# Performance work log

Measured on AMD Instinct MI355X. Metric: run time of the kernel, lower is better.

The kernel has to match this reference:

```python
import jax, jax.numpy as jnp
import numpy as np

DIM = 512
H = 4
HD = DIM // H
NPL = 2  # num_proj_layers
PS = float(np.sqrt(0.1))  # prior_strength ** 0.5


def conv1d(x, w, b):
    # x: [B,C,L], w: [O,I,3], SAME padding
    y = jax.lax.conv_general_dilated(x, w, window_strides=(1,), padding=[(1, 1)],
                                     dimension_numbers=('NCH', 'OIH', 'NCH'))
    return y + b[None, :, None]


def layernorm(x, g, b):
    m = jnp.mean(x, -1, keepdims=True)
    v = jnp.var(x, -1, keepdims=True)
    return (x - m) * jax.lax.rsqrt(v + 1e-5) * g + b


def maxpool1d(x):
    # kernel 3, stride 2, pad 1 (padded with -inf, matching torch MaxPool1d)
    return jax.lax.reduce_window(x, -jnp.inf, jax.lax.max, (1, 1, 3), (1, 1, 2),
                                 ((0, 0), (0, 0), (1, 1)))


def ds_block(x, cw, cb, g, b):
    # silu(conv) -> LN over channels -> maxpool; x: [B,C,L]
    x = jax.nn.silu(conv1d(x, cw, cb))
    x = jnp.swapaxes(layernorm(jnp.swapaxes(x, 1, 2), g, b), 1, 2)
    return maxpool1d(x)


def replicate_pad_odd(x):
    # F.pad(x, (0,0,0,1), 'replicate')[:, 1::2] on [B,S,D]
    return jnp.concatenate([x, x[:, -1:]], axis=1)[:, 1::2]


def setup_inputs() -> dict:
    key = jax.random.key(0)
    ks = jax.random.split(key, 16)
    B, Sq, Skv, C = 8, 2048, 512, DIM

    def n(k, shp, s=0.02):
        return jax.random.normal(k, shp, jnp.float32) * s

    return {
        'q_x': jax.random.normal(ks[0], (B, Sq, C), jnp.float32),
        'kv_x': jax.random.normal(ks[1], (B, Skv, C), jnp.float32),
        'q_freqs_cis': jax.random.normal(ks[2], (B, Sq, HD), jnp.float32),
        'k_freqs_cis': jax.random.normal(ks[3], (B, Skv, HD), jnp.float32),
        'mask': jnp.zeros((B, 1, (Sq + 1) // 2, Skv), jnp.float32),
        'attn_prior': jax.random.uniform(ks[4], (B, Sq, Skv), jnp.float32),
        'qds_conv_w': n(ks[5], (C, C, 3), 0.05),
        'qds_conv_b': jnp.zeros((C,), jnp.float32),
        'qds_ln_g': jnp.ones((C,), jnp.float32),
        'qds_ln_b': jnp.zeros((C,), jnp.float32),
        'qp_conv_w': n(ks[6], (NPL, C, C, 3), 0.05),
        'qp_conv_b': jnp.zeros((NPL, C), jnp.float32),
        'qp_ln_g': jnp.ones((NPL, C), jnp.float32),
        'qp_ln_b': jnp.zeros((NPL, C), jnp.float32),
        'wq': n(ks[7], (C, C)),
        'wk': n(ks[8], (C, C)),
        'wv': n(ks[9], (C, C)),
        'score_w': n(ks[10], (H, H, 45, 5), 0.02),
        'score_b': jnp.zeros((H,), jnp.float32),
        'proj_w': n(ks[11], (C, C)),
        'proj_b': jnp.zeros((C,), jnp.float32),
    }


def reference(q_x, kv_x, q_freqs_cis, k_freqs_cis, mask, attn_prior,
              qds_conv_w, qds_conv_b, qds_ln_g, qds_ln_b,
              qp_conv_w, qp_conv_b, qp_ln_g, qp_ln_b,
              wq, wk, wv, score_w, score_b, proj_w, proj_b):
    B, Sq, C = q_x.shape
    Skv = kv_x.shape[1]
    scale = HD ** -0.5

    # QueryDownsample: length Sq -> (Sq+1)//2
    x = ds_block(jnp.swapaxes(q_x, 1, 2), qds_conv_w, qds_conv_b, qds_ln_g, qds_ln_b)

    # QueryProj (note: original loop `for i in range(1, num_layers)` never uses xs[num_layers])
    xs = [x]
    for i in range(NPL):
        x = ds_block(x, qp_conv_w[i], qp_conv_b[i], qp_ln_g[i], qp_ln_b[i])
        xs.append(x)
    out = xs[0]
    for i in range(1, NPL):
        xi = jnp.repeat(xs[i], 2 ** i, axis=-1)  # nearest upsample
        out = out + xi[..., :out.shape[-1]]
    qx = jnp.swapaxes(out, 1, 2)  # [B, Sq2, C]
    Sq2 = (Sq + 1) // 2

    q = (qx @ wq.T).reshape(B, Sq2, H, HD)
    k = (kv_x @ wk.T).reshape(B, Skv, H, HD)
    v = (kv_x @ wv.T).reshape(B, Skv, H, HD)

    qf = replicate_pad_odd(q_freqs_cis)  # [B, Sq2, HD]
    q = q + qf[:, :, None] * PS
    k = k + k_freqs_cis[:, :, None] * PS

    q = jnp.swapaxes(q, 1, 2)  # [B,H,Sq2,HD]
    k = jnp.swapaxes(k, 1, 2)
    v = jnp.swapaxes(v, 1, 2)

    # gaussian attention: negative clamped squared L2 distance
    qs = q * scale
    kk = k * scale
    x2 = jnp.sum(qs * qs, -1)  # [B,H,Sq2]
    y2 = jnp.sum(kk * kk, -1)  # [B,H,Skv]
    xy = jnp.einsum('bhid,bhjd->bhij', qs, kk)
    attn = -jnp.clip(x2[..., :, None] + y2[..., None, :] - 2.0 * xy, 0.0, None)

    temp = jnp.linspace(1.0, 10.0, H).astype(attn.dtype)
    attn = attn / temp[None, :, None, None]

    # Conv2d(H,H,(45,5),padding=(22,2)) over the score map (mixes heads)
    sc = jax.lax.conv_general_dilated(attn, score_w, (1, 1), ((22, 22), (2, 2)),
                                      dimension_numbers=('NCHW', 'OIHW', 'NCHW'))
    attn = attn + sc + score_b[None, :, None, None]
    attn = attn + mask
    attn = jax.nn.softmax(attn, axis=-1)

    # prior log-fusion + renormalize
    prior = replicate_pad_odd(attn_prior)  # [B,Sq2,Skv]
    attn = jnp.exp(jnp.log(jnp.clip(attn, 1e-8, None)) +
                   jnp.log(jnp.clip(prior[:, None], 1e-8, None)))
    attn = attn / (jnp.sum(attn, -1, keepdims=True) + 1e-8)

    # nearest interpolate (Sq2 -> 2*Sq2) then crop to Sq
    attn = jnp.repeat(attn, 2, axis=2)[:, :, :Sq]  # [B,H,Sq,Skv]

    xout = jnp.einsum('bhqk,bhkd->bhqd', attn, v)
    xout = jnp.swapaxes(xout, 1, 2).reshape(B, Sq, C)
    xout = xout @ proj_w.T + proj_b
    return xout, attn
```

## Files before the change

### kernel.cpp

```cpp
#include <hip/hip_runtime.h>
#include <math.h>

#define PS_CONST 0.31622776601683794f

typedef __attribute__((ext_vector_type(8))) short short8;
typedef __attribute__((ext_vector_type(4))) float f32x4;

__device__ inline unsigned short f2b(float f) {
    unsigned u = __builtin_bit_cast(unsigned, f);
    unsigned r = (u + 0x7fffu + ((u >> 16) & 1u)) >> 16;
    return (unsigned short)r;
}

__global__ __launch_bounds__(256) void cvt_bf16_k(const float* __restrict__ in,
                                                  ushort* __restrict__ out, int n4)
{
    int idx = blockIdx.x * 256 + threadIdx.x;
    if (idx >= n4) return;
    float4 vv = ((const float4*)in)[idx];
    ushort4 o;
    o.x = f2b(vv.x); o.y = f2b(vv.y); o.z = f2b(vv.z); o.w = f2b(vv.w);
    ((ushort4*)out)[idx] = o;
}

__global__ __launch_bounds__(256) void wcvt_k(const float* __restrict__ w,
                                              ushort* __restrict__ out)
{
    int idx = blockIdx.x * 256 + threadIdx.x;
    if (idx >= 786432) return;
    int c = idx / 1536;
    int rem = idx - c * 1536;
    int tap = rem >> 9, i = rem & 511;
    out[idx] = f2b(w[c * 1536 + i * 3 + tap]);
}

__global__ __launch_bounds__(256) void wcvt4_k(
    const float* __restrict__ w0, const float* __restrict__ w1,
    const float* __restrict__ w2, const float* __restrict__ w3,
    ushort* __restrict__ o0, ushort* __restrict__ o1,
    ushort* __restrict__ o2, ushort* __restrict__ o3)
{
    int idx = blockIdx.x * 256 + threadIdx.x;
    int sel = idx >> 16, off = idx & 65535;
    const float* w = (sel == 0) ? w0 : (sel == 1) ? w1 : (sel == 2) ? w2 : w3;
    ushort* o = (sel == 0) ? o0 : (sel == 1) ? o1 : (sel == 2) ? o2 : o3;
    float4 vv = ((const float4*)w)[off];
    ushort4 r;
    r.x = f2b(vv.x); r.y = f2b(vv.y); r.z = f2b(vv.z); r.w = f2b(vv.w);
    ((ushort4*)o)[off] = r;
}

__global__ __launch_bounds__(256) void atoep_k(const float* __restrict__ sw,
                                               ushort* __restrict__ At)
{
    int idx = blockIdx.x * 256 + threadIdx.x;
    if (idx >= 81920) return;
    int t = idx & 7;
    int lane = (idx >> 3) & 63;
    int ks = (idx >> 9) & 1;
    int rem = idx >> 10;
    int dj = rem % 5, ohi = rem / 5;
    int m = lane & 15;
    int k = ks * 32 + ((lane >> 4) << 3) + t;
    int d = k - m;
    float val = (d >= 0 && d < 45) ? sw[(ohi * 45 + d) * 5 + dj] : 0.f;
    At[idx] = f2b(val);
}

__global__ __launch_bounds__(256) void conv_mfma(
    const ushort* __restrict__ xtb, const ushort* __restrict__ wtb,
    const float* __restrict__ cb, float* __restrict__ z, int L)
{
    __shared__ __align__(16) ushort Ash[128 * 40];
    __shared__ __align__(16) ushort Bsh[128 * 40];
    const int b = blockIdx.z;
    const int cm = blockIdx.y << 7;
    const int l0 = blockIdx.x << 7;
    const int tid = threadIdx.x;
    const int wave = tid >> 6, lane = tid & 63;
    const int wm = (wave & 1) << 6, wn = (wave >> 1) << 6;
    const int lo16 = lane & 15, hi4 = lane >> 4;

    f32x4 acc[4][4];
    #pragma unroll
    for (int i = 0; i < 4; i++)
        #pragma unroll
        for (int j = 0; j < 4; j++)
            acc[i][j] = (f32x4){0.f, 0.f, 0.f, 0.f};

    for (int k0 = 0; k0 < 1536; k0 += 32) {
        const int tap = k0 >> 9;
        const int cbase = k0 & 511;
        {
            int u = tid;
            #pragma unroll
            for (int p = 0; p < 2; p++, u += 256) {
                int row = u >> 2, g = (u & 3) << 3;
                *(uint4*)&Ash[row * 40 + g] =
                    *(const uint4*)&wtb[(size_t)(cm + row) * 1536 + k0 + g];
            }
        }
        {
            int u = tid;
            #pragma unroll
            for (int p = 0; p < 2; p++, u += 256) {
                int row = u >> 2, g = (u & 3) << 3;
                int lg = l0 + tap - 1 + row;
                uint4 val = make_uint4(0u, 0u, 0u, 0u);
                if (lg >= 0 && lg < L)
                    val = *(const uint4*)&xtb[((size_t)b * L + lg) * 512 + cbase + g];
                *(uint4*)&Bsh[row * 40 + g] = val;
            }
        }
        __syncthreads();
        short8 a[4], bb[4];
        #pragma unroll
        for (int t = 0; t < 4; t++) {
            a[t]  = *(const short8*)&Ash[(wm + t * 16 + lo16) * 40 + hi4 * 8];
            bb[t] = *(const short8*)&Bsh[(wn + t * 16 + lo16) * 40 + hi4 * 8];
        }
        #pragma unroll
        for (int mt = 0; mt < 4; mt++)
            #pragma unroll
            for (int nt = 0; nt < 4; nt++)
                acc[mt][nt] = __builtin_amdgcn_mfma_f32_16x16x32_bf16(
                    a[mt], bb[nt], acc[mt][nt], 0, 0, 0);
        __syncthreads();
    }
    #pragma unroll
    for (int mt = 0; mt < 4; mt++) {
        #pragma unroll
        for (int r = 0; r < 4; r++) {
            int c = cm + wm + mt * 16 + hi4 * 4 + r;
            float bias = cb[c];
            #pragma unroll
            for (int nt = 0; nt < 4; nt++) {
                int l = l0 + wn + nt * 16 + lo16;
                float u = acc[mt][nt][r] + bias;
                u = u / (1.f + __expf(-u));
                z[((size_t)b * 512 + c) * L + l] = u;
            }
        }
    }
}

__global__ __launch_bounds__(256) void gemm_mfma_bf16(
    const ushort* __restrict__ Xb, const ushort* __restrict__ Wb,
    const float* __restrict__ bias, float* __restrict__ Y,
    int M, int N, int K, int dup)
{
    __shared__ __align__(16) ushort Ash[128 * 40];
    __shared__ __align__(16) ushort Bsh[128 * 40];
    const int bm = blockIdx.y << 7, bn = blockIdx.x << 7;
    const int tid = threadIdx.x;
    const int wave = tid >> 6, lane = tid & 63;
    const int wm = (wave & 1) << 6, wn = (wave >> 1) << 6;
    const int lo16 = lane & 15, hi4 = lane >> 4;

    f32x4 acc[4][4];
    #pragma unroll
    for (int i = 0; i < 4; i++)
        #pragma unroll
        for (int j = 0; j < 4; j++)
            acc[i][j] = (f32x4){0.f, 0.f, 0.f, 0.f};

    for (int k0 = 0; k0 < K; k0 += 32) {
        int u = tid;
        #pragma unroll
        for (int p = 0; p < 2; p++, u += 256) {
            int row = u >> 2, g = (u & 3) << 3;
            *(uint4*)&Ash[row * 40 + g] =
                *(const uint4*)&Xb[(size_t)(bm + row) * K + k0 + g];
            *(uint4*)&Bsh[row * 40 + g] =
                *(const uint4*)&Wb[(size_t)(bn + row) * K + k0 + g];
        }
        __syncthreads();
        short8 a[4], bb[4];
        #pragma unroll
        for (int t = 0; t < 4; t++) {
            a[t]  = *(const short8*)&Ash[(wm + t * 16 + lo16) * 40 + hi4 * 8];
            bb[t] = *(const short8*)&Bsh[(wn + t * 16 + lo16) * 40 + hi4 * 8];
        }
        #pragma unroll
        for (int mt = 0; mt < 4; mt++)
            #pragma unroll
            for (int nt = 0; nt < 4; nt++)
                acc[mt][nt] = __builtin_amdgcn_mfma_f32_16x16x32_bf16(
                    a[mt], bb[nt], acc[mt][nt], 0, 0, 0);
        __syncthreads();
    }
    #pragma unroll
    for (int mt = 0; mt < 4; mt++) {
        #pragma unroll
        for (int r = 0; r < 4; r++) {
            int m = bm + wm + mt * 16 + hi4 * 4 + r;
            #pragma unroll
            for (int nt = 0; nt < 4; nt++) {
                int n = bn + wn + nt * 16 + lo16;
                float val = acc[mt][nt][r];
                if (bias) val += bias[n];
                if (dup) {
                    Y[(size_t)(2 * m)     * N + n] = val;
                    Y[(size_t)(2 * m + 1) * N + n] = val;
                } else {
                    Y[(size_t)m * N + n] = val;
                }
            }
        }
    }
}

__global__ __launch_bounds__(256) void ln_stats_k(const float* __restrict__ z,
                                                  float2* __restrict__ stats, int L)
{
    __shared__ float s_sh[4][64];
    __shared__ float s2_sh[4][64];
    const int b = blockIdx.y;
    const int colL = threadIdx.x & 63;
    const int col = (blockIdx.x << 6) + colL;
    const int part = threadIdx.x >> 6;
    const float* base = z + ((size_t)b * 512 + part * 128) * L + col;
    float s = 0.f, s2 = 0.f;
    for (int i = 0; i < 128; i++) {
        float vv = base[(size_t)i * L];
        s += vv; s2 += vv * vv;
    }
    s_sh[part][colL] = s; s2_sh[part][colL] = s2;
    __syncthreads();
    if (threadIdx.x < 64) {
        float ts = 0.f, ts2 = 0.f;
        #pragma unroll
        for (int p = 0; p < 4; p++) { ts += s_sh[p][colL]; ts2 += s2_sh[p][colL]; }
        float m = ts * (1.f / 512.f);
        float var = ts2 * (1.f / 512.f) - m * m;
        stats[(size_t)b * L + col] = make_float2(m, rsqrtf(var + 1e-5f));
    }
}

__global__ __launch_bounds__(256) void ln_maxpool_k(
    const float* __restrict__ z, const float2* __restrict__ stats,
    const float* __restrict__ g, const float* __restrict__ be,
    float* __restrict__ out, int L, int lshift)
{
    const int Lout = 1 << lshift;
    size_t idx = (size_t)blockIdx.x * 256 + threadIdx.x;
    int lp = (int)(idx & (Lout - 1));
    int c = (int)((idx >> lshift) & 511);
    int b = (int)(idx >> (lshift + 9));
    const float* zp = z + ((size_t)b * 512 + c) * L;
    const float2* sp = stats + (size_t)b * L;
    float gc = g[c], bc = be[c];
    int l = lp << 1;
    float2 st = sp[l];
    float m = (zp[l] - st.x) * st.y * gc + bc;
    if (l > 0) {
        float2 s0 = sp[l - 1];
        m = fmaxf(m, (zp[l - 1] - s0.x) * s0.y * gc + bc);
    }
    float2 s1 = sp[l + 1];
    m = fmaxf(m, (zp[l + 1] - s1.x) * s1.y * gc + bc);
    out[idx] = m;
}

__global__ __launch_bounds__(256) void transpose_cvt_k(const float* __restrict__ x0,
                                                       ushort* __restrict__ xtb)
{
    __shared__ ushort t[32][33];
    const int b = blockIdx.z, c0 = blockIdx.y << 5, l0 = blockIdx.x << 5;
    const int col = threadIdx.x & 31, r0 = threadIdx.x >> 5;
    #pragma unroll
    for (int p = 0; p < 4; p++) {
        int r = r0 + p * 8;
        t[r][col] = f2b(x0[((size_t)b * 512 + c0 + r) * 1024 + l0 + col]);
    }
    __syncthreads();
    #pragma unroll
    for (int p = 0; p < 4; p++) {
        int r = r0 + p * 8;
        xtb[((size_t)b * 1024 + l0 + r) * 512 + c0 + col] = t[col][r];
    }
}

__global__ __launch_bounds__(256) void vT_cvt_k(const float* __restrict__ v,
                                                ushort* __restrict__ vTb)
{
    __shared__ ushort t[32][33];
    const int bh = blockIdx.z, b = bh >> 2, h = bh & 3;
    const int d0 = blockIdx.y << 5, j0 = blockIdx.x << 5;
    const int col = threadIdx.x & 31, r0 = threadIdx.x >> 5;
    #pragma unroll
    for (int p = 0; p < 4; p++) {
        int r = r0 + p * 8;
        t[r][col] = f2b(v[(((size_t)b * 512 + j0 + r) * 4 + h) * 128 + d0 + col]);
    }
    __syncthreads();
    #pragma unroll
    for (int p = 0; p < 4; p++) {
        int r = r0 + p * 8;
        vTb[((size_t)bh * 128 + d0 + r) * 512 + j0 + col] = t[col][r];
    }
}

__global__ __launch_bounds__(256) void upsample_add_t(const float* __restrict__ x0,
    const float* __restrict__ x1, ushort* __restrict__ qxb)
{
    size_t idx = (size_t)blockIdx.x * 256 + threadIdx.x;
    int c = (int)(idx & 511);
    int l = (int)((idx >> 9) & 1023);
    int b = (int)(idx >> 19);
    qxb[idx] = f2b(x0[((size_t)b * 512 + c) * 1024 + l] +
                   x1[((size_t)b * 512 + c) * 512 + (l >> 1)]);
}

__global__ __launch_bounds__(256) void add_freq_q_k(float* __restrict__ q, const float* __restrict__ qf)
{
    size_t idx = (size_t)blockIdx.x * 256 + threadIdx.x;
    int d = (int)(idx & 127);
    int l = (int)((idx >> 9) & 1023);
    int b = (int)(idx >> 19);
    q[idx] += PS_CONST * qf[((size_t)b * 2048 + 2 * l + 1) * 128 + d];
}

__global__ __launch_bounds__(256) void add_freq_k_k(float* __restrict__ k, const float* __restrict__ kf)
{
    size_t idx = (size_t)blockIdx.x * 256 + threadIdx.x;
    int d = (int)(idx & 127);
    int j = (int)((idx >> 9) & 511);
    int b = (int)(idx >> 18);
    k[idx] += PS_CONST * kf[((size_t)b * 512 + j) * 128 + d];
}

__global__ __launch_bounds__(64) void rownorm_k(const float* __restrict__ X,
                                                float* __restrict__ out, int Li)
{
    int i = blockIdx.x, bh = blockIdx.y;
    int b = bh >> 2, h = bh & 3;
    const float* row = X + (((size_t)b * Li + i) * 4 + h) * 128;
    int lane = threadIdx.x;
    float v0 = row[lane], v1 = row[lane + 64];
    float s = v0 * v0 + v1 * v1;
    #pragma unroll
    for (int off = 32; off > 0; off >>= 1) s += __shfl_down(s, off);
    if (lane == 0) out[(size_t)bh * Li + i] = s;
}

__global__ __launch_bounds__(256) void scores_k(
    const float* __restrict__ q, const float* __restrict__ k,
    const float* __restrict__ q2, const float* __restrict__ k2,
    float* __restrict__ attn0)
{
    __shared__ float As[16][68];
    __shared__ float Bs[16][68];
    const int bh = blockIdx.z, b = bh >> 2, h = bh & 3;
    const float* A  = q + (size_t)b * (1024 * 512) + h * 128;
    const float* Bm = k + (size_t)b * (512 * 512) + h * 128;
    const int bm = blockIdx.y << 6, bn = blockIdx.x << 6;
    const int tx = threadIdx.x & 15, ty = threadIdx.x >> 4;
    const int lrow = threadIdx.x >> 2, lkc = (threadIdx.x & 3) << 2;
    float acc[4][4] = {};
    for (int k0 = 0; k0 < 128; k0 += 16) {
        float4 a4 = *(const float4*)&A[(size_t)(bm + lrow) * 512 + k0 + lkc];
        float4 b4 = *(const float4*)&Bm[(size_t)(bn + lrow) * 512 + k0 + lkc];
        As[lkc+0][lrow] = a4.x; As[lkc+1][lrow] = a4.y; As[lkc+2][lrow] = a4.z; As[lkc+3][lrow] = a4.w;
        Bs[lkc+0][lrow] = b4.x; Bs[lkc+1][lrow] = b4.y; Bs[lkc+2][lrow] = b4.z; Bs[lkc+3][lrow] = b4.w;
        __syncthreads();
        #pragma unroll
        for (int kk = 0; kk < 16; kk++) {
            float4 a4v = *(const float4*)&As[kk][ty << 2];
            float4 b4v = *(const float4*)&Bs[kk][tx << 2];
            float a[4] = {a4v.x, a4v.y, a4v.z, a4v.w};
            float bb[4] = {b4v.x, b4v.y, b4v.z, b4v.w};
            #pragma unroll
            for (int u = 0; u < 4; u++)
                #pragma unroll
                for (int vv = 0; vv < 4; vv++)
                    acc[u][vv] = fmaf(a[u], bb[vv], acc[u][vv]);
        }
        __syncthreads();
    }
    const float it = (h == 0) ? 1.f : (h == 1) ? 0.25f : (h == 2) ? (1.f / 7.f) : 0.1f;
    float* orow = attn0 + (size_t)bh * (1024 * 512);
    #pragma unroll
    for (int u = 0; u < 4; u++) {
        int i = bm + (ty << 2) + u;
        float q2v = q2[(size_t)bh * 1024 + i];
        #pragma unroll
        for (int vv = 0; vv < 4; vv++) {
            int j = bn + (tx << 2) + vv;
            float d2 = q2v + k2[(size_t)bh * 512 + j] - 2.f * acc[u][vv];
            d2 *= (1.f / 128.f);
            if (d2 < 0.f) d2 = 0.f;
            orow[(size_t)i * 512 + j] = -d2 * it;
        }
    }
}

__global__ __launch_bounds__(256) void score_conv_mfma(
    const float* __restrict__ attn0, const ushort* __restrict__ At,
    const float* __restrict__ sb, const float* __restrict__ mask,
    float* __restrict__ attn1)
{
    __shared__ __align__(16) ushort tileT[4 * 68 * 120];
    const int b = blockIdx.z, i0 = blockIdx.y << 6, j0 = blockIdx.x << 6;
    const int tid = threadIdx.x, wave = tid >> 6, lane = tid & 63;

    for (int idx = tid; idx < 4 * 68 * 56; idx += 256) {
        int jj = idx % 68;
        int r2 = idx / 68;
        int ip = r2 % 56, hi = r2 / 56;
        int ii = ip << 1;
        int gi = i0 - 22 + ii, gj = j0 - 2 + jj;
        const float* src = attn0 + ((size_t)(b * 4 + hi) * 1024 + gi) * 512 + gj;
        bool jv = (unsigned)gj < 512u;
        float v0 = (jv && (unsigned)gi       < 1024u) ? src[0]   : 0.f;
        float v1 = (jv && (unsigned)(gi + 1) < 1024u) ? src[512] : 0.f;
        unsigned pk = (unsigned)f2b(v0) | ((unsigned)f2b(v1) << 16);
        *(unsigned*)&tileT[(hi * 68 + jj) * 120 + ii] = pk;
    }
    __syncthreads();

    const int n16 = lane & 15, quad = lane >> 4;
    f32x4 acc[4][4];
    #pragma unroll
    for (int o = 0; o < 4; o++)
        #pragma unroll
        for (int t = 0; t < 4; t++)
            acc[o][t] = (f32x4){0.f, 0.f, 0.f, 0.f};

    const int iibase = wave * 16 + quad * 8;
    #pragma unroll 1
    for (int hi = 0; hi < 4; hi++) {
        #pragma unroll 1
        for (int dj = 0; dj < 5; dj++) {
            #pragma unroll
            for (int ks = 0; ks < 2; ks++) {
                short8 bf[4];
                #pragma unroll
                for (int t = 0; t < 4; t++)
                    bf[t] = *(const short8*)&tileT[(hi * 68 + t * 16 + n16 + dj) * 120
                                                   + iibase + ks * 32];
                #pragma unroll
                for (int o = 0; o < 4; o++) {
                    short8 af = *(const short8*)&At[((((o * 4 + hi) * 5 + dj) * 2 + ks) * 64
                                                     + lane) * 8];
                    #pragma unroll
                    for (int t = 0; t < 4; t++)
                        acc[o][t] = __builtin_amdgcn_mfma_f32_16x16x32_bf16(
                            af, bf[t], acc[o][t], 0, 0, 0);
                }
            }
        }
    }

    #pragma unroll
    for (int o = 0; o < 4; o++) {
        float bo = sb[o];
        #pragma unroll
        for (int r = 0; r < 4; r++) {
            int i = i0 + wave * 16 + quad * 4 + r;
            size_t obase = ((size_t)(b * 4 + o) * 1024 + i) * 512;
            size_t mbase = ((size_t)b * 1024 + i) * 512;
            #pragma unroll
            for (int t = 0; t < 4; t++) {
                int j = j0 + t * 16 + n16;
                attn1[obase + j] = attn0[obase + j] + acc[o][t][r] + bo + mask[mbase + j];
            }
        }
    }
}

__global__ __launch_bounds__(256) void softmax_prior_k(
    const float* __restrict__ attn1, const float* __restrict__ prior,
    float* __restrict__ attn_out)
{
    const int wid = threadIdx.x >> 6, lane = threadIdx.x & 63;
    size_t row = (size_t)blockIdx.x * 4 + wid;
    int i = (int)(row & 1023);
    int bh = (int)(row >> 10);
    int b = bh >> 2;
    const float* arow = attn1 + row * 512;
    const float* prow = prior + ((size_t)b * 2048 + 2 * i + 1) * 512;
    float v[8], p[8];
    #pragma unroll
    for (int t = 0; t < 8; t++) {
        v[t] = arow[lane + 64 * t];
        p[t] = prow[lane + 64 * t];
    }
    float mx = v[0];
    #pragma unroll
    for (int t = 1; t < 8; t++) mx = fmaxf(mx, v[t]);
    #pragma unroll
    for (int off = 32; off > 0; off >>= 1) mx = fmaxf(mx, __shfl_xor(mx, off));
    float sum = 0.f;
    #pragma unroll
    for (int t = 0; t < 8; t++) { v[t] = expf(v[t] - mx); sum += v[t]; }
    #pragma unroll
    for (int off = 32; off > 0; off >>= 1) sum += __shfl_xor(sum, off);
    float inv = 1.f / sum;
    float sum2 = 0.f;
    #pragma unroll
    for (int t = 0; t < 8; t++) {
        float sm = fmaxf(v[t] * inv, 1e-8f);
        float pr = fmaxf(p[t], 1e-8f);
        v[t] = sm * pr;
        sum2 += v[t];
    }
    #pragma unroll
    for (int off = 32; off > 0; off >>= 1) sum2 += __shfl_xor(sum2, off);
    float inv2 = 1.f / (sum2 + 1e-8f);
    float* o0 = attn_out + ((size_t)bh * 2048 + 2 * i) * 512;
    #pragma unroll
    for (int t = 0; t < 8; t++) {
        float val = v[t] * inv2;
        o0[lane + 64 * t] = val;
        o0[512 + lane + 64 * t] = val;
    }
}

__global__ __launch_bounds__(256) void attnv_mfma(
    const float* __restrict__ attn, const ushort* __restrict__ vTb,
    ushort* __restrict__ xpb)
{
    __shared__ __align__(16) ushort Ash[128 * 40];
    __shared__ __align__(16) ushort Bsh[128 * 40];
    const int bh = blockIdx.z, b = bh >> 2, h = bh & 3;
    const int bm = blockIdx.y << 7;
    const float* A = attn + (size_t)bh * 2048 * 512;
    const ushort* B = vTb + (size_t)bh * 128 * 512;
    const int tid = threadIdx.x;
    const int wave = tid >> 6, lane = tid & 63;
    const int wm = (wave & 1) << 6, wn = (wave >> 1) << 6;
    const int lo16 = lane & 15, hi4 = lane >> 4;

    f32x4 acc[4][4];
    #pragma unroll
    for (int i = 0; i < 4; i++)
        #pragma unroll
        for (int j = 0; j < 4; j++)
            acc[i][j] = (f32x4){0.f, 0.f, 0.f, 0.f};

    for (int k0 = 0; k0 < 512; k0 += 32) {
        int u = tid;
        #pragma unroll
        for (int p = 0; p < 2; p++, u += 256) {
            int row = u >> 2, g = (u & 3) << 3;
            const float* ap = &A[(size_t)(2 * (bm + row)) * 512 + k0 + g];
            float4 f0 = *(const float4*)ap;
            float4 f1 = *(const float4*)(ap + 4);
            ushort4 p0, p1;
            p0.x = f2b(f0.x); p0.y = f2b(f0.y); p0.z = f2b(f0.z); p0.w = f2b(f0.w);
            p1.x = f2b(f1.x); p1.y = f2b(f1.y); p1.z = f2b(f1.z); p1.w = f2b(f1.w);
            *(ushort4*)&Ash[row * 40 + g]     = p0;
            *(ushort4*)&Ash[row * 40 + g + 4] = p1;
            *(uint4*)&Bsh[row * 40 + g] = *(const uint4*)&B[(size_t)row * 512 + k0 + g];
        }
        __syncthreads();
        short8 a[4], bb[4];
        #pragma unroll
        for (int t = 0; t < 4; t++) {
            a[t]  = *(const short8*)&Ash[(wm + t * 16 + lo16) * 40 + hi4 * 8];
            bb[t] = *(const short8*)&Bsh[(wn + t * 16 + lo16) * 40 + hi4 * 8];
        }
        #pragma unroll
        for (int mt = 0; mt < 4; mt++)
            #pragma unroll
            for (int nt = 0; nt < 4; nt++)
                acc[mt][nt] = __builtin_amdgcn_mfma_f32_16x16x32_bf16(
                    a[mt], bb[nt], acc[mt][nt], 0, 0, 0);
        __syncthreads();
    }
    #pragma unroll
    for (int mt = 0; mt < 4; mt++) {
        #pragma unroll
        for (int r = 0; r < 4; r++) {
            int m = bm + wm + mt * 16 + hi4 * 4 + r;
            #pragma unroll
            for (int nt = 0; nt < 4; nt++) {
                int n = wn + nt * 16 + lo16;
                xpb[((size_t)b * 1024 + m) * 512 + h * 128 + n] = f2b(acc[mt][nt][r]);
            }
        }
    }
}

extern "C" void kernel_launch(void* const* d_in, const int* in_sizes, int n_in,
                              void* d_out, int out_size, void* d_ws, size_t ws_size,
                              hipStream_t stream)
{
    const float* q_x    = (const float*)d_in[0];
    const float* kv_x   = (const float*)d_in[1];
    const float* qf     = (const float*)d_in[2];
    const float* kf     = (const float*)d_in[3];
    const float* mask   = (const float*)d_in[4];
    const float* prior  = (const float*)d_in[5];
    const float* qds_w  = (const float*)d_in[6];
    const float* qds_b  = (const float*)d_in[7];
    const float* qds_g  = (const float*)d_in[8];
    const float* qds_be = (const float*)d_in[9];
    const float* qp_w   = (const float*)d_in[10];
    const float* qp_b   = (const float*)d_in[11];
    const float* qp_g   = (const float*)d_in[12];
    const float* qp_be  = (const float*)d_in[13];
    const float* wq     = (const float*)d_in[14];
    const float* wk     = (const float*)d_in[15];
    const float* wv     = (const float*)d_in[16];
    const float* sw     = (const float*)d_in[17];
    const float* sb     = (const float*)d_in[18];
    const float* pw     = (const float*)d_in[19];
    const float* pb     = (const float*)d_in[20];

    if (ws_size < (size_t)56672256 * 4) return;
    float* ws = (float*)d_ws;
    float* z     = ws;
    float* x0    = ws + 8388608;
    float* x1    = ws + 12582912;
    float* q     = ws + 14680064;
    float* k     = ws + 18874368;
    float* v     = ws + 20971520;
    float* q2    = ws + 23068672;
    float* k2    = ws + 23101440;
    float* attn0 = ws + 23117824;
    float* attn1 = ws + 39895040;
    ushort* xtb   = (ushort*)(ws + 39895040);
    ushort* x0tb  = (ushort*)(ws + 39895040 + 4194304);
    ushort* wc1b  = (ushort*)(ws + 39895040 + 6291456);
    ushort* wc2b  = (ushort*)(ws + 39895040 + 6684672);
    float2* stats1 = (float2*)(ws + 39895040 + 7077888);
    float2* stats2 = (float2*)(ws + 39895040 + 7110656);
    ushort* qxb  = (ushort*)z;
    ushort* At   = (ushort*)x0;
    ushort* wqb  = (ushort*)(ws + 8454144);
    ushort* wkb  = (ushort*)(ws + 8585216);
    ushort* wvb  = (ushort*)(ws + 8716288);
    ushort* pwb  = (ushort*)(ws + 8847360);
    ushort* vTb  = (ushort*)(ws + 11010048);
    ushort* kvb  = (ushort*)x1;
    ushort* xpb  = (ushort*)attn0;

    float* out_x    = (float*)d_out;
    float* out_attn = out_x + (size_t)8 * 2048 * 512;

    cvt_bf16_k<<<8192, 256, 0, stream>>>(q_x, xtb, 2097152);
    wcvt_k<<<3072, 256, 0, stream>>>(qds_w, wc1b);
    wcvt_k<<<3072, 256, 0, stream>>>(qp_w, wc2b);
    conv_mfma<<<dim3(16, 4, 8), 256, 0, stream>>>(xtb, wc1b, qds_b, z, 2048);
    ln_stats_k<<<dim3(32, 8), 256, 0, stream>>>(z, stats1, 2048);
    ln_maxpool_k<<<16384, 256, 0, stream>>>(z, stats1, qds_g, qds_be, x0, 2048, 10);
    transpose_cvt_k<<<dim3(32, 16, 8), 256, 0, stream>>>(x0, x0tb);
    conv_mfma<<<dim3(8, 4, 8), 256, 0, stream>>>(x0tb, wc2b, qp_b, z, 1024);
    ln_stats_k<<<dim3(16, 8), 256, 0, stream>>>(z, stats2, 1024);
    ln_maxpool_k<<<8192, 256, 0, stream>>>(z, stats2, qp_g, qp_be, x1, 1024, 9);
    upsample_add_t<<<16384, 256, 0, stream>>>(x0, x1, qxb);
    atoep_k<<<320, 256, 0, stream>>>(sw, At);
    wcvt4_k<<<1024, 256, 0, stream>>>(wq, wk, wv, pw, wqb, wkb, wvb, pwb);
    cvt_bf16_k<<<2048, 256, 0, stream>>>(kv_x, kvb, 524288);
    gemm_mfma_bf16<<<dim3(4, 64), 256, 0, stream>>>(qxb, wqb, nullptr, q, 8192, 512, 512, 0);
    gemm_mfma_bf16<<<dim3(4, 32), 256, 0, stream>>>(kvb, wkb, nullptr, k, 4096, 512, 512, 0);
    gemm_mfma_bf16<<<dim3(4, 32), 256, 0, stream>>>(kvb, wvb, nullptr, v, 4096, 512, 512, 0);
    add_freq_q_k<<<16384, 256, 0, stream>>>(q, qf);
    add_freq_k_k<<<8192, 256, 0, stream>>>(k, kf);
    rownorm_k<<<dim3(1024, 32), 64, 0, stream>>>(q, q2, 1024);
    rownorm_k<<<dim3(512, 32), 64, 0, stream>>>(k, k2, 512);
    vT_cvt_k<<<dim3(16, 4, 32), 256, 0, stream>>>(v, vTb);
    scores_k<<<dim3(8, 16, 32), 256, 0, stream>>>(q, k, q2, k2, attn0);
    score_conv_mfma<<<dim3(8, 16, 8), 256, 0, stream>>>(attn0, At, sb, mask, attn1);
    softmax_prior_k<<<8192, 256, 0, stream>>>(attn1, prior, out_attn);
    attnv_mfma<<<dim3(1, 8, 32), 256, 0, stream>>>(out_attn, vTb, xpb);
    gemm_mfma_bf16<<<dim3(4, 64), 256, 0, stream>>>(xpb, pwb, pb, out_x, 8192, 512, 512, 1);
}
```

Baseline: 786.5 us.

## Compute distance scores with split-bf16 MFMA instead of scalar FP32 GEMM

```diff
diff --git a/kernel.cpp b/kernel.cpp
--- a/kernel.cpp
+++ b/kernel.cpp
@@ -10,6 +10,9 @@
     unsigned u = __builtin_bit_cast(unsigned, f);
     unsigned r = (u + 0x7fffu + ((u >> 16) & 1u)) >> 16;
     return (unsigned short)r;
+}
+__device__ inline float b2f(unsigned short b) {
+    return __builtin_bit_cast(float, (unsigned)b << 16);
 }
 
 __global__ __launch_bounds__(256) void cvt_bf16_k(const float* __restrict__ in,
@@ -21,6 +24,23 @@
     ushort4 o;
     o.x = f2b(vv.x); o.y = f2b(vv.y); o.z = f2b(vv.z); o.w = f2b(vv.w);
     ((ushort4*)out)[idx] = o;
+}
+
+__global__ __launch_bounds__(256) void split_bf16_k(const float* __restrict__ in,
+    ushort* __restrict__ hi, ushort* __restrict__ lo, int n4)
+{
+    int idx = blockIdx.x * 256 + threadIdx.x;
+    if (idx >= n4) return;
+    float4 vv = ((const float4*)in)[idx];
+    float vs[4] = {vv.x, vv.y, vv.z, vv.w};
+    ushort4 h, l;
+    unsigned short hb; float hf;
+    hb = f2b(vs[0]); hf = b2f(hb); h.x = hb; l.x = f2b(vs[0] - hf);
+    hb = f2b(vs[1]); hf = b2f(hb); h.y = hb; l.y = f2b(vs[1] - hf);
+    hb = f2b(vs[2]); hf = b2f(hb); h.z = hb; l.z = f2b(vs[2] - hf);
+    hb = f2b(vs[3]); hf = b2f(hb); h.w = hb; l.w = f2b(vs[3] - hf);
+    ((ushort4*)hi)[idx] = h;
+    ((ushort4*)lo)[idx] = l;
 }
 
 __global__ __launch_bounds__(256) void wcvt_k(const float* __restrict__ w,
@@ -344,53 +364,81 @@
     if (lane == 0) out[(size_t)bh * Li + i] = s;
 }
 
-__global__ __launch_bounds__(256) void scores_k(
-    const float* __restrict__ q, const float* __restrict__ k,
+__global__ __launch_bounds__(256) void scores_mfma(
+    const ushort* __restrict__ qhi, const ushort* __restrict__ qlo,
+    const ushort* __restrict__ khi, const ushort* __restrict__ klo,
     const float* __restrict__ q2, const float* __restrict__ k2,
     float* __restrict__ attn0)
 {
-    __shared__ float As[16][68];
-    __shared__ float Bs[16][68];
+    __shared__ __align__(16) ushort Ah[128 * 40];
+    __shared__ __align__(16) ushort Al[128 * 40];
+    __shared__ __align__(16) ushort Bh[128 * 40];
+    __shared__ __align__(16) ushort Bl[128 * 40];
     const int bh = blockIdx.z, b = bh >> 2, h = bh & 3;
-    const float* A  = q + (size_t)b * (1024 * 512) + h * 128;
-    const float* Bm = k + (size_t)b * (512 * 512) + h * 128;
-    const int bm = blockIdx.y << 6, bn = blockIdx.x << 6;
-    const int tx = threadIdx.x & 15, ty = threadIdx.x >> 4;
-    const int lrow = threadIdx.x >> 2, lkc = (threadIdx.x & 3) << 2;
-    float acc[4][4] = {};
-    for (int k0 = 0; k0 < 128; k0 += 16) {
-        float4 a4 = *(const float4*)&A[(size_t)(bm + lrow) * 512 + k0 + lkc];
-        float4 b4 = *(const float4*)&Bm[(size_t)(bn + lrow) * 512 + k0 + lkc];
-        As[lkc+0][lrow] = a4.x; As[lkc+1][lrow] = a4.y; As[lkc+2][lrow] = a4.z; As[lkc+3][lrow] = a4.w;
-        Bs[lkc+0][lrow] = b4.x; Bs[lkc+1][lrow] = b4.y; Bs[lkc+2][lrow] = b4.z; Bs[lkc+3][lrow] = b4.w;
+    const int bm = blockIdx.y << 7, bn = blockIdx.x << 7;
+    const int tid = threadIdx.x;
+    const int wave = tid >> 6, lane = tid & 63;
+    const int wm = (wave & 1) << 6, wn = (wave >> 1) << 6;
+    const int lo16 = lane & 15, hi4 = lane >> 4;
+
+    f32x4 acc[4][4];
+    #pragma unroll
+    for (int i = 0; i < 4; i++)
+        #pragma unroll
+        for (int j = 0; j < 4; j++)
+            acc[i][j] = (f32x4){0.f, 0.f, 0.f, 0.f};
+
+    for (int k0 = 0; k0 < 128; k0 += 32) {
+        int u = tid;
+        #pragma unroll
+        for (int p = 0; p < 2; p++, u += 256) {
+            int row = u >> 2, g = (u & 3) << 3;
+            size_t aoff = (((size_t)b * 1024 + bm + row) * 4 + h) * 128 + k0 + g;
+            size_t boff = (((size_t)b * 512  + bn + row) * 4 + h) * 128 + k0 + g;
+            *(uint4*)&Ah[row * 40 + g] = *(const uint4*)&qhi[aoff];
+            *(uint4*)&Al[row * 40 + g] = *(const uint4*)&qlo[aoff];
+            *(uint4*)&Bh[row * 40 + g] = *(const uint4*)&khi[boff];
+            *(uint4*)&Bl[row * 40 + g] = *(const uint4*)&klo[boff];
+        }
         __syncthreads();
-        #pragma unroll
-        for (int kk = 0; kk < 16; kk++) {
-            float4 a4v = *(const float4*)&As[kk][ty << 2];
-            float4 b4v = *(const float4*)&Bs[kk][tx << 2];
-            float a[4] = {a4v.x, a4v.y, a4v.z, a4v.w};
-            float bb[4] = {b4v.x, b4v.y, b4v.z, b4v.w};
-            #pragma unroll
-            for (int u = 0; u < 4; u++)
-                #pragma unroll
-                for (int vv = 0; vv < 4; vv++)
-                    acc[u][vv] = fmaf(a[u], bb[vv], acc[u][vv]);
-        }
+        short8 ah[4], al[4], bhF[4], blF[4];
+        #pragma unroll
+        for (int t = 0; t < 4; t++) {
+            int ar = (wm + t * 16 + lo16) * 40 + hi4 * 8;
+            int br = (wn + t * 16 + lo16) * 40 + hi4 * 8;
+            ah[t]  = *(const short8*)&Ah[ar];
+            al[t]  = *(const short8*)&Al[ar];
+            bhF[t] = *(const short8*)&Bh[br];
+            blF[t] = *(const short8*)&Bl[br];
+        }
+        #pragma unroll
+        for (int mt = 0; mt < 4; mt++)
+            #pragma unroll
+            for (int nt = 0; nt < 4; nt++) {
+                acc[mt][nt] = __builtin_amdgcn_mfma_f32_16x16x32_bf16(
+                    ah[mt], bhF[nt], acc[mt][nt], 0, 0, 0);
+                acc[mt][nt] = __builtin_amdgcn_mfma_f32_16x16x32_bf16(
+                    ah[mt], blF[nt], acc[mt][nt], 0, 0, 0);
+                acc[mt][nt] = __builtin_amdgcn_mfma_f32_16x16x32_bf16(
+                    al[mt], bhF[nt], acc[mt][nt], 0, 0, 0);
+            }
         __syncthreads();
     }
     const float it = (h == 0) ? 1.f : (h == 1) ? 0.25f : (h == 2) ? (1.f / 7.f) : 0.1f;
-    float* orow = attn0 + (size_t)bh * (1024 * 512);
-    #pragma unroll
-    for (int u = 0; u < 4; u++) {
-        int i = bm + (ty << 2) + u;
-        float q2v = q2[(size_t)bh * 1024 + i];
-        #pragma unroll
-        for (int vv = 0; vv < 4; vv++) {
-            int j = bn + (tx << 2) + vv;
-            float d2 = q2v + k2[(size_t)bh * 512 + j] - 2.f * acc[u][vv];
-            d2 *= (1.f / 128.f);
-            if (d2 < 0.f) d2 = 0.f;
-            orow[(size_t)i * 512 + j] = -d2 * it;
+    #pragma unroll
+    for (int mt = 0; mt < 4; mt++) {
+        #pragma unroll
+        for (int r = 0; r < 4; r++) {
+            int i = bm + wm + mt * 16 + hi4 * 4 + r;
+            float q2v = q2[(size_t)bh * 1024 + i];
+            #pragma unroll
+            for (int nt = 0; nt < 4; nt++) {
+                int j = bn + wn + nt * 16 + lo16;
+                float d2 = q2v + k2[(size_t)bh * 512 + j] - 2.f * acc[mt][nt][r];
+                d2 *= (1.f / 128.f);
+                if (d2 < 0.f) d2 = 0.f;
+                attn0[((size_t)bh * 1024 + i) * 512 + j] = -d2 * it;
+            }
         }
     }
 }
@@ -633,8 +681,12 @@
     ushort* wkb  = (ushort*)(ws + 8585216);
     ushort* wvb  = (ushort*)(ws + 8716288);
     ushort* pwb  = (ushort*)(ws + 8847360);
-    ushort* vTb  = (ushort*)(ws + 11010048);
+    ushort* khi  = (ushort*)(ws + 8978432);
+    ushort* klo  = (ushort*)(ws + 10027008);
+    ushort* vTb  = (ushort*)(ws + 11075584);
     ushort* kvb  = (ushort*)x1;
+    ushort* qhi  = (ushort*)z;
+    ushort* qlo  = (ushort*)(ws + 2097152);
     ushort* xpb  = (ushort*)attn0;
 
     float* out_x    = (float*)d_out;
@@ -661,8 +713,10 @@
     add_freq_k_k<<<8192, 256, 0, stream>>>(k, kf);
     rownorm_k<<<dim3(1024, 32), 64, 0, stream>>>(q, q2, 1024);
     rownorm_k<<<dim3(512, 32), 64, 0, stream>>>(k, k2, 512);
+    split_bf16_k<<<4096, 256, 0, stream>>>(q, qhi, qlo, 1048576);
+    split_bf16_k<<<2048, 256, 0, stream>>>(k, khi, klo, 524288);
     vT_cvt_k<<<dim3(16, 4, 32), 256, 0, stream>>>(v, vTb);
-    scores_k<<<dim3(8, 16, 32), 256, 0, stream>>>(q, k, q2, k2, attn0);
+    scores_mfma<<<dim3(4, 8, 32), 256, 0, stream>>>(qhi, qlo, khi, klo, q2, k2, attn0);
     score_conv_mfma<<<dim3(8, 16, 8), 256, 0, stream>>>(attn0, At, sb, mask, attn1);
     softmax_prior_k<<<8192, 256, 0, stream>>>(attn1, prior, out_attn);
     attnv_mfma<<<dim3(1, 8, 32), 256, 0, stream>>>(out_attn, vTb, xpb);
```

Measured after the change: 771.1 us. About the same (-2.0%).
